# Performance work log

Hardware: AMD Instinct MI355X
Metric: run time of the kernel (lower is better)

The kernel has to match this reference:

```python
import jax, jax.numpy as jnp
import numpy as np

N = 100000      # nodes
E = 1600000     # edges (avg degree 16)
F_IN = 128      # num_node_features
H = 64          # hidden_features
C = 40          # num_classes


def _glorot(key, shape):
    lim = np.sqrt(6.0 / (shape[0] + shape[1]))
    return jax.random.uniform(key, shape, jnp.float32, -lim, lim)


def setup_inputs() -> dict:
    key = jax.random.key(0)
    k = jax.random.split(key, 4)
    x = jax.random.normal(k[0], (N, F_IN), dtype=jnp.float32)
    edge_index = jax.random.randint(k[1], (2, E), 0, N, dtype=jnp.int32)
    W1 = _glorot(k[2], (F_IN, H))
    b1 = jnp.zeros((H,), jnp.float32)
    W2 = _glorot(k[3], (H, C))
    b2 = jnp.zeros((C,), jnp.float32)
    return {"x": x, "edge_index": edge_index, "W1": W1, "b1": b1, "W2": W2, "b2": b2}


def _gcn_conv(x, src, dst, dinv_sqrt, W, b):
    # GCNConv: out = D^{-1/2} (A + I) D^{-1/2} (x W) + b
    h = x @ W                                        # [N, out]
    norm = dinv_sqrt[src] * dinv_sqrt[dst]           # [E+N]
    msg = h[src] * norm[:, None]                     # gather + scale
    agg = jax.ops.segment_sum(msg, dst, num_segments=N)
    return agg + b


def reference(x, edge_index, W1, b1, W2, b2):
    loop = jnp.arange(N, dtype=edge_index.dtype)
    src = jnp.concatenate([edge_index[0], loop])     # add self-loops
    dst = jnp.concatenate([edge_index[1], loop])
    # degree of A + I (counts in-edges at destination, incl. self-loop)
    deg = jax.ops.segment_sum(jnp.ones_like(dst, jnp.float32), dst, num_segments=N)
    dinv_sqrt = jax.lax.rsqrt(deg)                   # deg >= 1 due to self-loops

    h = _gcn_conv(x, src, dst, dinv_sqrt, W1, b1)
    h = jax.nn.relu(h)
    # F.dropout(training=self.training) is identity in eval mode
    out = _gcn_conv(h, src, dst, dinv_sqrt, W2, b2)
    return out
```

## Files before the change

### kernel.cpp

```cpp
#include <hip/hip_runtime.h>
#include <hip/hip_fp16.h>
#include <cstdint>
#include <cstddef>

#define NPB_SHIFT 8
#define NPB (1 << NPB_SHIFT)
#define CHUNK 4096
#define BCHUNK 8192

typedef _Float16 half8_t __attribute__((ext_vector_type(8)));
typedef _Float16 half4_t __attribute__((ext_vector_type(4)));
typedef float floatx4 __attribute__((ext_vector_type(4)));

__device__ inline float ush2f(unsigned short u) {
  __half_raw r; r.x = u;
  return __half2float(__half(r));
}
__device__ inline void h8f(uint4 v, float* f) {
  f[0] = ush2f((unsigned short)(v.x & 0xffff)); f[1] = ush2f((unsigned short)(v.x >> 16));
  f[2] = ush2f((unsigned short)(v.y & 0xffff)); f[3] = ush2f((unsigned short)(v.y >> 16));
  f[4] = ush2f((unsigned short)(v.z & 0xffff)); f[5] = ush2f((unsigned short)(v.z >> 16));
  f[6] = ush2f((unsigned short)(v.w & 0xffff)); f[7] = ush2f((unsigned short)(v.w >> 16));
}


__global__ __launch_bounds__(256) void k_bcount(const int* __restrict__ dst,
                                                int* __restrict__ btot, int E, int nbuck) {
  __shared__ int cnt[512];
  int tid = threadIdx.x;
  for (int i = tid; i < nbuck; i += 256) cnt[i] = 0;
  __syncthreads();
  int base = blockIdx.x * BCHUNK;
  int end = min(base + BCHUNK, E);
  for (int e = base + tid; e < end; e += 256) atomicAdd(&cnt[dst[e] >> NPB_SHIFT], 1);
  __syncthreads();
  for (int i = tid; i < nbuck; i += 256)
    if (cnt[i]) atomicAdd(&btot[i], cnt[i]);
}

__global__ void k_bscan(const int* __restrict__ btot, int* __restrict__ bbase,
                        int* __restrict__ bfill, int nbuck, int E) {
  __shared__ int tmp[512];
  int tid = threadIdx.x;
  int v = (tid < nbuck) ? btot[tid] : 0;
  tmp[tid] = v;
  __syncthreads();
  for (int off = 1; off < 512; off <<= 1) {
    int t = (tid >= off) ? tmp[tid - off] : 0;
    __syncthreads();
    tmp[tid] += t;
    __syncthreads();
  }
  if (tid < nbuck) { int ex = tmp[tid] - v; bbase[tid] = ex; bfill[tid] = ex; }
  if (tid == 0) bbase[nbuck] = E;
}

__global__ __launch_bounds__(256) void k_partition(const int* __restrict__ src,
                                                   const int* __restrict__ dst,
                                                   int* __restrict__ bfill,
                                                   unsigned* __restrict__ tmp,
                                                   int E, int nbuck) {
  __shared__ int cnt[512];
  __shared__ int base[512];
  __shared__ int cur[512];
  int tid = threadIdx.x;
  int cbase = blockIdx.x * CHUNK;
  for (int i = tid; i < nbuck; i += 256) { cnt[i] = 0; cur[i] = 0; }
  __syncthreads();
  int s[16], d[16];
  bool valid[16];
#pragma unroll
  for (int u = 0; u < 16; ++u) {
    int e = cbase + u * 256 + tid;
    valid[u] = e < E;
    s[u] = valid[u] ? src[e] : 0;
    d[u] = valid[u] ? dst[e] : 0;
    if (valid[u]) atomicAdd(&cnt[d[u] >> NPB_SHIFT], 1);
  }
  __syncthreads();
  for (int i = tid; i < nbuck; i += 256)
    if (cnt[i]) base[i] = atomicAdd(&bfill[i], cnt[i]);
  __syncthreads();
#pragma unroll
  for (int u = 0; u < 16; ++u) {
    if (valid[u]) {
      int b = d[u] >> NPB_SHIFT;
      int r = atomicAdd(&cur[b], 1);
      tmp[base[b] + r] = ((unsigned)s[u] << NPB_SHIFT) | (unsigned)(d[u] & (NPB - 1));
    }
  }
}

__global__ __launch_bounds__(256) void k_csr_build(const unsigned* __restrict__ tmp,
                                                   const int* __restrict__ bbase,
                                                   float* __restrict__ dinv,
                                                   int* __restrict__ offset,
                                                   int* __restrict__ ssrc,
                                                   int N, int E, int nbuck) {
  __shared__ int cnt[NPB];
  __shared__ int scan[NPB];
  __shared__ int fillL[NPB];
  int b = blockIdx.x, tid = threadIdx.x;
  int nbase = b << NPB_SHIFT;
  int nloc = min(NPB, N - nbase);
  cnt[tid] = 0;
  __syncthreads();
  int ebeg = bbase[b], eend = bbase[b + 1];
  for (int j = ebeg + tid; j < eend; j += 256) atomicAdd(&cnt[tmp[j] & (NPB - 1)], 1);
  __syncthreads();
  int v = cnt[tid];
  scan[tid] = v;
  __syncthreads();
  for (int off = 1; off < NPB; off <<= 1) {
    int t = (tid >= off) ? scan[tid - off] : 0;
    __syncthreads();
    scan[tid] += t;
    __syncthreads();
  }
  int myoff = ebeg + scan[tid] - v;
  fillL[tid] = myoff;
  if (tid < nloc) {
    offset[nbase + tid] = myoff;
    dinv[nbase + tid] = rsqrtf((float)(v + 1));
  }
  if (b == nbuck - 1 && tid == 0) offset[N] = E;
  __syncthreads();
  int j = ebeg + tid;
  for (; j + 3 * 256 < eend; j += 4 * 256) {
    unsigned p[4];
#pragma unroll
    for (int u = 0; u < 4; ++u) p[u] = tmp[j + u * 256];
#pragma unroll
    for (int u = 0; u < 4; ++u) {
      int pos = atomicAdd(&fillL[p[u] & (NPB - 1)], 1);
      ssrc[pos] = (int)(p[u] >> NPB_SHIFT);
    }
  }
  for (; j < eend; j += 256) {
    unsigned p = tmp[j];
    int pos = atomicAdd(&fillL[p & (NPB - 1)], 1);
    ssrc[pos] = (int)(p >> NPB_SHIFT);
  }
}

template <int K, int COLS, int MT, int KC, int OS>
__global__ __launch_bounds__(256) void k_gemm_mfma(const float* __restrict__ x,
                                                   const float* __restrict__ W,
                                                   const float* __restrict__ dinv,
                                                   _Float16* __restrict__ out, int n) {
  int lane = threadIdx.x & 63;
  int quad = lane >> 4;
  int l15 = lane & 15;
  int gwave = (blockIdx.x * blockDim.x + threadIdx.x) >> 6;
  int nwave = (gridDim.x * blockDim.x) >> 6;
  int ntiles = (n + 15) >> 4;

  half8_t afrag[MT][KC];
#pragma unroll
  for (int m = 0; m < MT; ++m) {
    int colw = m * 16 + l15;
    if (colw > COLS - 1) colw = COLS - 1;
#pragma unroll
    for (int c = 0; c < KC; ++c) {
#pragma unroll
      for (int j = 0; j < 8; ++j) {
        int kk = c * 32 + quad * 8 + j;
        afrag[m][c][j] = (_Float16)W[kk * COLS + colw];
      }
    }
  }

  for (int tile = gwave; tile < ntiles; tile += nwave) {
    int node0 = tile << 4;
    int nodeB = node0 + l15;
    int nodeC = nodeB < n ? nodeB : n - 1;
    const float* xr = x + (size_t)nodeC * K;
    float dv = dinv[nodeC];
    half8_t bfrag[KC];
#pragma unroll
    for (int c = 0; c < KC; ++c) {
      float4 lo = *(const float4*)(xr + c * 32 + quad * 8);
      float4 hi = *(const float4*)(xr + c * 32 + quad * 8 + 4);
      bfrag[c][0] = (_Float16)lo.x; bfrag[c][1] = (_Float16)lo.y;
      bfrag[c][2] = (_Float16)lo.z; bfrag[c][3] = (_Float16)lo.w;
      bfrag[c][4] = (_Float16)hi.x; bfrag[c][5] = (_Float16)hi.y;
      bfrag[c][6] = (_Float16)hi.z; bfrag[c][7] = (_Float16)hi.w;
    }
    floatx4 acc[MT];
#pragma unroll
    for (int m = 0; m < MT; ++m) acc[m] = (floatx4){0.f, 0.f, 0.f, 0.f};
#pragma unroll
    for (int c = 0; c < KC; ++c)
#pragma unroll
      for (int m = 0; m < MT; ++m)
        acc[m] = __builtin_amdgcn_mfma_f32_16x16x32_f16(afrag[m][c], bfrag[c], acc[m], 0, 0, 0);

    if (nodeB < n) {
#pragma unroll
      for (int m = 0; m < MT; ++m) {
        int colBase = m * 16 + quad * 4;
        if (colBase < COLS) {
          half4_t hv = {(_Float16)(acc[m][0] * dv), (_Float16)(acc[m][1] * dv),
                        (_Float16)(acc[m][2] * dv), (_Float16)(acc[m][3] * dv)};
          *(half4_t*)(out + (size_t)nodeB * OS + colBase) = hv;
        }
      }
    }
  }
}

template <int F, int S8, bool RELU>
__global__ __launch_bounds__(256) void k_agg_v8(const uint4* __restrict__ h8,
                                                const int* __restrict__ offset,
                                                const int* __restrict__ ssrc,
                                                const float* __restrict__ dinv,
                                                const float* __restrict__ bias,
                                                float* __restrict__ outp, int n) {
  constexpr int F8 = F / 8;
  int lane = threadIdx.x & 63;
  int g = lane >> 3;
  int t = lane & 7;
  int node = (blockIdx.x * blockDim.x + threadIdx.x) >> 6;
  if (node >= n) return;
  bool tv = t < F8;
  float di = dinv[node];
  float acc[8];
#pragma unroll
  for (int i = 0; i < 8; ++i) acc[i] = 0.f;

  if (g == 0 && tv) {
    float v[8];
    h8f(h8[(size_t)node * S8 + t], v);
#pragma unroll
    for (int i = 0; i < 8; ++i) acc[i] = v[i];
  }

  int beg = offset[node], end = offset[node + 1];
  int j = beg;
  for (; j + 16 <= end; j += 16) {
    int sA = ssrc[j + g];
    int sB = ssrc[j + 8 + g];
    uint4 rA = tv ? h8[(size_t)sA * S8 + t] : make_uint4(0, 0, 0, 0);
    uint4 rB = tv ? h8[(size_t)sB * S8 + t] : make_uint4(0, 0, 0, 0);
    float vA[8], vB[8];
    h8f(rA, vA); h8f(rB, vB);
#pragma unroll
    for (int i = 0; i < 8; ++i) acc[i] += vA[i] + vB[i];
  }
  for (; j + 8 <= end; j += 8) {
    int s = ssrc[j + g];
    uint4 rv = tv ? h8[(size_t)s * S8 + t] : make_uint4(0, 0, 0, 0);
    float v[8];
    h8f(rv, v);
#pragma unroll
    for (int i = 0; i < 8; ++i) acc[i] += v[i];
  }
  if (j < end) {
    int r = end - j;
    int gi = (g < r) ? g : (r - 1);
    int s = ssrc[j + gi];
    uint4 rv = (tv && g < r) ? h8[(size_t)s * S8 + t] : make_uint4(0, 0, 0, 0);
    float v[8];
    h8f(rv, v);
#pragma unroll
    for (int i = 0; i < 8; ++i) acc[i] += v[i];
  }

#pragma unroll
  for (int i = 0; i < 8; ++i) acc[i] += __shfl_xor(acc[i], 8);
#pragma unroll
  for (int i = 0; i < 8; ++i) acc[i] += __shfl_xor(acc[i], 16);
#pragma unroll
  for (int i = 0; i < 8; ++i) acc[i] += __shfl_xor(acc[i], 32);

  if (lane < F8) {
    const float* bb = bias + lane * 8;
    float4 r0 = make_float4(fmaf(acc[0], di, bb[0]), fmaf(acc[1], di, bb[1]),
                            fmaf(acc[2], di, bb[2]), fmaf(acc[3], di, bb[3]));
    float4 r1 = make_float4(fmaf(acc[4], di, bb[4]), fmaf(acc[5], di, bb[5]),
                            fmaf(acc[6], di, bb[6]), fmaf(acc[7], di, bb[7]));
    if (RELU) {
      r0.x = fmaxf(r0.x, 0.f); r0.y = fmaxf(r0.y, 0.f);
      r0.z = fmaxf(r0.z, 0.f); r0.w = fmaxf(r0.w, 0.f);
      r1.x = fmaxf(r1.x, 0.f); r1.y = fmaxf(r1.y, 0.f);
      r1.z = fmaxf(r1.z, 0.f); r1.w = fmaxf(r1.w, 0.f);
    }
    float4* o4 = (float4*)(outp + (size_t)node * F + lane * 8);
    o4[0] = r0; o4[1] = r1;
  }
}


extern "C" void kernel_launch(void* const* d_in, const int* in_sizes, int n_in,
                              void* d_out, int out_size, void* d_ws, size_t ws_size,
                              hipStream_t stream) {
  const float* x  = (const float*)d_in[0];
  const int*   ei = (const int*)d_in[1];
  const float* W1 = (const float*)d_in[2];
  const float* b1 = (const float*)d_in[3];
  const float* W2 = (const float*)d_in[4];
  const float* b2 = (const float*)d_in[5];
  float* out = (float*)d_out;

  const int F_IN = 128, HID = 64, C = 40;
  int N = in_sizes[0] / F_IN;
  int E = in_sizes[1] / 2;
  const int* src = ei;
  const int* dst = ei + E;
  int nbuck = (N + NPB - 1) >> NPB_SHIFT;

  char* w = (char*)d_ws;
  size_t o = 0;
  auto alloc = [&](size_t bytes) -> void* {
    void* p = w + o;
    o = (o + bytes + 255) & ~(size_t)255;
    return p;
  };
  float*    dinv   = (float*)alloc((size_t)N * 4);
  int*      offset = (int*)alloc((size_t)(N + 1) * 4);
  int*      btot   = (int*)alloc(512 * 4);
  int*      bbase  = (int*)alloc(513 * 4);
  int*      bfill  = (int*)alloc(512 * 4);
  unsigned* tmp    = (unsigned*)alloc((size_t)E * 4);
  int*      ssrc   = (int*)alloc((size_t)E * 4);
  _Float16* g1     = (_Float16*)alloc((size_t)N * HID * 2);
  float*    h1     = (float*)alloc((size_t)N * HID * 4);
  _Float16* g2     = (_Float16*)alloc((size_t)N * C * 2);

  dim3 b256(256);

  hipMemsetAsync(btot, 0, 512 * 4, stream);
  k_bcount<<<dim3((E + BCHUNK - 1) / BCHUNK), b256, 0, stream>>>(dst, btot, E, nbuck);
  k_bscan<<<dim3(1), dim3(512), 0, stream>>>(btot, bbase, bfill, nbuck, E);

  k_partition<<<dim3((E + CHUNK - 1) / CHUNK), b256, 0, stream>>>(src, dst, bfill, tmp, E, nbuck);
  k_csr_build<<<dim3(nbuck), b256, 0, stream>>>(tmp, bbase, dinv, offset, ssrc, N, E, nbuck);

  k_gemm_mfma<128, 64, 4, 4, 64><<<dim3(256), b256, 0, stream>>>(x, W1, dinv, g1, N);
  k_agg_v8<64, 8, true><<<dim3((N + 3) / 4), b256, 0, stream>>>(
      (const uint4*)g1, offset, ssrc, dinv, b1, h1, N);

  k_gemm_mfma<64, 40, 3, 2, 40><<<dim3(256), b256, 0, stream>>>(h1, W2, dinv, g2, N);
  k_agg_v8<40, 5, false><<<dim3((N + 3) / 4), b256, 0, stream>>>(
      (const uint4*)g2, offset, ssrc, dinv, b2, out, N);
}
```

Baseline: 269.7 us.

## Accumulate aggregation in packed fp16 and stage partition writes in LDS

The aggregation kernel now accumulates the gathered fp16 neighbour features in packed half2 registers, including the cross-lane shuffle reduction, instead of converting each element to fp32. This removes the per-element conversion work and halves register use for the accumulators. The cost is lower accumulation precision and a risk of fp16 overflow or rounding error. Separately, the partition kernel scans its local bucket counts, sorts each chunk's edges into shared memory by bucket, and then writes them out in a contiguous pass, replacing scattered global stores with more coalesced ones.

```diff
diff --git a/kernel.cpp b/kernel.cpp
--- a/kernel.cpp
+++ b/kernel.cpp
@@ -10,18 +10,10 @@
 
 typedef _Float16 half8_t __attribute__((ext_vector_type(8)));
 typedef _Float16 half4_t __attribute__((ext_vector_type(4)));
+typedef _Float16 half2_t __attribute__((ext_vector_type(2)));
 typedef float floatx4 __attribute__((ext_vector_type(4)));
 
-__device__ inline float ush2f(unsigned short u) {
-  __half_raw r; r.x = u;
-  return __half2float(__half(r));
-}
-__device__ inline void h8f(uint4 v, float* f) {
-  f[0] = ush2f((unsigned short)(v.x & 0xffff)); f[1] = ush2f((unsigned short)(v.x >> 16));
-  f[2] = ush2f((unsigned short)(v.y & 0xffff)); f[3] = ush2f((unsigned short)(v.y >> 16));
-  f[4] = ush2f((unsigned short)(v.z & 0xffff)); f[5] = ush2f((unsigned short)(v.z >> 16));
-  f[6] = ush2f((unsigned short)(v.w & 0xffff)); f[7] = ush2f((unsigned short)(v.w >> 16));
-}
+#define H2(u) __builtin_bit_cast(half2_t, (u))
 
 
 __global__ __launch_bounds__(256) void k_bcount(const int* __restrict__ dst,
@@ -61,11 +53,15 @@
                                                    unsigned* __restrict__ tmp,
                                                    int E, int nbuck) {
   __shared__ int cnt[512];
-  __shared__ int base[512];
+  __shared__ int lbase[512];
+  __shared__ int gdelta[512];
   __shared__ int cur[512];
+  __shared__ int ps[256];
+  __shared__ unsigned sval[CHUNK];
+  __shared__ unsigned short sbid[CHUNK];
   int tid = threadIdx.x;
   int cbase = blockIdx.x * CHUNK;
-  for (int i = tid; i < nbuck; i += 256) { cnt[i] = 0; cur[i] = 0; }
+  for (int i = tid; i < 512; i += 256) cnt[i] = 0;
   __syncthreads();
   int s[16], d[16];
   bool valid[16];
@@ -78,16 +74,40 @@
     if (valid[u]) atomicAdd(&cnt[d[u] >> NPB_SHIFT], 1);
   }
   __syncthreads();
-  for (int i = tid; i < nbuck; i += 256)
-    if (cnt[i]) base[i] = atomicAdd(&bfill[i], cnt[i]);
+  int c0 = cnt[2 * tid], c1 = cnt[2 * tid + 1];
+  int p = c0 + c1;
+  ps[tid] = p;
+  __syncthreads();
+  for (int off = 1; off < 256; off <<= 1) {
+    int t = (tid >= off) ? ps[tid - off] : 0;
+    __syncthreads();
+    ps[tid] += t;
+    __syncthreads();
+  }
+  int ep = ps[tid] - p;
+  lbase[2 * tid] = ep;
+  lbase[2 * tid + 1] = ep + c0;
+  __syncthreads();
+  for (int i = tid; i < 512; i += 256) {
+    cur[i] = lbase[i];
+    if (cnt[i]) gdelta[i] = atomicAdd(&bfill[i], cnt[i]) - lbase[i];
+  }
   __syncthreads();
 #pragma unroll
   for (int u = 0; u < 16; ++u) {
     if (valid[u]) {
       int b = d[u] >> NPB_SHIFT;
       int r = atomicAdd(&cur[b], 1);
-      tmp[base[b] + r] = ((unsigned)s[u] << NPB_SHIFT) | (unsigned)(d[u] & (NPB - 1));
-    }
+      sval[r] = ((unsigned)s[u] << NPB_SHIFT) | (unsigned)(d[u] & (NPB - 1));
+      sbid[r] = (unsigned short)b;
+    }
+  }
+  __syncthreads();
+  int nv = min(CHUNK, E - cbase);
+  for (int i = tid; i < nv; i += 256) {
+    unsigned v = sval[i];
+    int b = sbid[i];
+    tmp[gdelta[b] + i] = v;
   }
 }
 
@@ -224,15 +244,13 @@
   if (node >= n) return;
   bool tv = t < F8;
   float di = dinv[node];
-  float acc[8];
-#pragma unroll
-  for (int i = 0; i < 8; ++i) acc[i] = 0.f;
+  half2_t acc[4];
+#pragma unroll
+  for (int k = 0; k < 4; ++k) acc[k] = H2(0u);
 
   if (g == 0 && tv) {
-    float v[8];
-    h8f(h8[(size_t)node * S8 + t], v);
-#pragma unroll
-    for (int i = 0; i < 8; ++i) acc[i] = v[i];
+    uint4 v = h8[(size_t)node * S8 + t];
+    acc[0] += H2(v.x); acc[1] += H2(v.y); acc[2] += H2(v.z); acc[3] += H2(v.w);
   }
 
   int beg = offset[node], end = offset[node + 1];
@@ -242,43 +260,44 @@
     int sB = ssrc[j + 8 + g];
     uint4 rA = tv ? h8[(size_t)sA * S8 + t] : make_uint4(0, 0, 0, 0);
     uint4 rB = tv ? h8[(size_t)sB * S8 + t] : make_uint4(0, 0, 0, 0);
-    float vA[8], vB[8];
-    h8f(rA, vA); h8f(rB, vB);
-#pragma unroll
-    for (int i = 0; i < 8; ++i) acc[i] += vA[i] + vB[i];
+    acc[0] += H2(rA.x); acc[1] += H2(rA.y); acc[2] += H2(rA.z); acc[3] += H2(rA.w);
+    acc[0] += H2(rB.x); acc[1] += H2(rB.y); acc[2] += H2(rB.z); acc[3] += H2(rB.w);
   }
   for (; j + 8 <= end; j += 8) {
     int s = ssrc[j + g];
     uint4 rv = tv ? h8[(size_t)s * S8 + t] : make_uint4(0, 0, 0, 0);
-    float v[8];
-    h8f(rv, v);
-#pragma unroll
-    for (int i = 0; i < 8; ++i) acc[i] += v[i];
+    acc[0] += H2(rv.x); acc[1] += H2(rv.y); acc[2] += H2(rv.z); acc[3] += H2(rv.w);
   }
   if (j < end) {
     int r = end - j;
     int gi = (g < r) ? g : (r - 1);
     int s = ssrc[j + gi];
     uint4 rv = (tv && g < r) ? h8[(size_t)s * S8 + t] : make_uint4(0, 0, 0, 0);
-    float v[8];
-    h8f(rv, v);
-#pragma unroll
-    for (int i = 0; i < 8; ++i) acc[i] += v[i];
-  }
-
-#pragma unroll
-  for (int i = 0; i < 8; ++i) acc[i] += __shfl_xor(acc[i], 8);
-#pragma unroll
-  for (int i = 0; i < 8; ++i) acc[i] += __shfl_xor(acc[i], 16);
-#pragma unroll
-  for (int i = 0; i < 8; ++i) acc[i] += __shfl_xor(acc[i], 32);
+    acc[0] += H2(rv.x); acc[1] += H2(rv.y); acc[2] += H2(rv.z); acc[3] += H2(rv.w);
+  }
+
+#pragma unroll
+  for (int k = 0; k < 4; ++k) {
+    int u = __builtin_bit_cast(int, acc[k]);
+    acc[k] += H2((unsigned)__shfl_xor(u, 8));
+    u = __builtin_bit_cast(int, acc[k]);
+    acc[k] += H2((unsigned)__shfl_xor(u, 16));
+    u = __builtin_bit_cast(int, acc[k]);
+    acc[k] += H2((unsigned)__shfl_xor(u, 32));
+  }
 
   if (lane < F8) {
+    float f[8];
+#pragma unroll
+    for (int k = 0; k < 4; ++k) {
+      f[2 * k] = (float)acc[k][0];
+      f[2 * k + 1] = (float)acc[k][1];
+    }
     const float* bb = bias + lane * 8;
-    float4 r0 = make_float4(fmaf(acc[0], di, bb[0]), fmaf(acc[1], di, bb[1]),
-                            fmaf(acc[2], di, bb[2]), fmaf(acc[3], di, bb[3]));
-    float4 r1 = make_float4(fmaf(acc[4], di, bb[4]), fmaf(acc[5], di, bb[5]),
-                            fmaf(acc[6], di, bb[6]), fmaf(acc[7], di, bb[7]));
+    float4 r0 = make_float4(fmaf(f[0], di, bb[0]), fmaf(f[1], di, bb[1]),
+                            fmaf(f[2], di, bb[2]), fmaf(f[3], di, bb[3]));
+    float4 r1 = make_float4(fmaf(f[4], di, bb[4]), fmaf(f[5], di, bb[5]),
+                            fmaf(f[6], di, bb[6]), fmaf(f[7], di, bb[7]));
     if (RELU) {
       r0.x = fmaxf(r0.x, 0.f); r0.y = fmaxf(r0.y, 0.f);
       r0.z = fmaxf(r0.z, 0.f); r0.w = fmaxf(r0.w, 0.f);
```

New measurement: 264.8 us. Within noise of the previous version (-1.8%).
